# Optimization experiments

Measured on AMD Instinct MI355X. Metric: run time of the kernel, lower is better.

## Reference

```python
import jax, jax.numpy as jnp
import numpy as np

BLOCK_SIZE = 128
N_OUT = 4096
K_IN = 4096


def setup_inputs() -> dict:
    key = jax.random.key(0)
    k_x, k_w, k_s = jax.random.split(key, 3)
    x = jax.random.normal(k_x, (1, 1024, K_IN), dtype=jnp.float32)
    # ternary weights stored as int8 in {-2,-1,0,+1} (zero-point subtracted)
    weight_q = (jax.random.randint(k_w, (N_OUT, K_IN), 0, 4) - 2).astype(jnp.int8)
    n_blocks = K_IN // BLOCK_SIZE
    scales = jax.random.uniform(k_s, (N_OUT, n_blocks), dtype=jnp.float32) * 0.1 + 0.01
    return {"x": x, "weight_q": weight_q, "scales": scales}


def reference(x, weight_q, scales):
    N, K = weight_q.shape
    n_blocks = K // BLOCK_SIZE
    orig_shape = x.shape
    # [tokens, n_blocks, block_size]
    x_blocked = x.reshape(-1, n_blocks, BLOCK_SIZE).astype(jnp.float32)
    # [N, n_blocks, block_size]
    w_blocked = weight_q.reshape(N, n_blocks, BLOCK_SIZE).astype(jnp.float32)
    # per-block partial dot products: [tokens, N, n_blocks]
    raw = jnp.einsum('bki,nki->bnk', x_blocked, w_blocked)
    # apply per-(out_feature, block) scale then reduce over blocks
    out = (raw * scales).sum(axis=-1)  # [tokens, N]
    return out.astype(x.dtype).reshape(*orig_shape[:-1], N)
```

## Files before the change

kernel.cpp:

```cpp
#include <hip/hip_runtime.h>
#include <stdint.h>


#define MM 1024
#define NN 4096
#define KK 4096
#define BK 128

typedef __attribute__((ext_vector_type(4))) int intx4;
typedef __attribute__((ext_vector_type(4))) float floatx4;

typedef const __attribute__((address_space(1))) void global_cvoid;
typedef __attribute__((address_space(3))) void lds_void;

__global__ __launch_bounds__(256) void quant_x(const float* __restrict__ x,
                                               char* __restrict__ xq,
                                               float* __restrict__ qrow) {
    const int m   = blockIdx.x;
    const int tid = threadIdx.x;
    const float* xr = x + (size_t)m * KK;
    floatx4 v[4];
    float amax = 0.f;
#pragma unroll
    for (int c = 0; c < 4; ++c) {
        v[c] = *(const floatx4*)(xr + (c * 256 + tid) * 4);
#pragma unroll
        for (int e = 0; e < 4; ++e) amax = fmaxf(amax, fabsf(v[c][e]));
    }
#pragma unroll
    for (int off = 32; off; off >>= 1) amax = fmaxf(amax, __shfl_down(amax, off));
    __shared__ float wmax[4];
    if ((tid & 63) == 0) wmax[tid >> 6] = amax;
    __syncthreads();
    amax = fmaxf(fmaxf(wmax[0], wmax[1]), fmaxf(wmax[2], wmax[3]));
    amax = fmaxf(amax, 1e-20f);
    const float qinv = 127.0f / amax;
    if (tid == 0) qrow[m] = amax / 127.0f;
#pragma unroll
    for (int c = 0; c < 4; ++c) {
        int p = 0;
#pragma unroll
        for (int e = 0; e < 4; ++e) {
            float r = rintf(v[c][e] * qinv);
            r = fminf(fmaxf(r, -127.f), 127.f);
            p |= ((int)r & 255) << (8 * e);
        }
        *(int*)(xq + (size_t)m * KK + (c * 256 + tid) * 4) = p;
    }
}

__global__ __launch_bounds__(256) void conv_w8(const int* __restrict__ wq,
                                               char* __restrict__ wb) {
    int t = blockIdx.x * 256 + threadIdx.x;
    const intx4* src = (const intx4*)wq + (size_t)t * 4;
    intx4 o;
#pragma unroll
    for (int c = 0; c < 4; ++c) {
        intx4 a = src[c];
        o[c] = (a[0] & 255) | ((a[1] & 255) << 8) | ((a[2] & 255) << 16) | (a[3] << 24);
    }
    *((intx4*)wb + t) = o;
}

__global__ __launch_bounds__(256) void q8_gemm(const char* __restrict__ xq,
                                               const char* __restrict__ wb,
                                               const float* __restrict__ qrow,
                                               const float* __restrict__ scales,
                                               float* __restrict__ out) {
    __shared__ char As[2][128 * BK];
    __shared__ char Bs[2][128 * BK];
    __shared__ float Sl[32 * 128];

    const int tid  = threadIdx.x;
    const int lane = tid & 63;
    const int wave = tid >> 6;
    const int wm   = (wave & 1) * 64;
    const int wn   = (wave >> 1) * 64;
    const int r16  = lane & 15;
    const int quad = lane >> 4;
    const int sw   = r16 & 7;

    const int bid = blockIdx.x;
    const int xcd = bid & 7, loc = bid >> 3;
    const int nT = xcd * 4 + (loc & 3);
    const int mT = loc >> 2;
    const int mBase = mT * 128, nBase = nT * 128;

    const int rg = lane >> 3;
    const int cs = (lane & 7) ^ rg;
    const char* gA = xq + (size_t)(mBase + wave * 32 + rg) * KK + cs * 16;
    const char* gB = wb + (size_t)(nBase + wave * 32 + rg) * KK + cs * 16;
    const int ldsRow = wave * 32;

    floatx4 facc[4][4];
#pragma unroll
    for (int i = 0; i < 4; ++i)
#pragma unroll
        for (int j = 0; j < 4; ++j) facc[i][j] = (floatx4){0.f, 0.f, 0.f, 0.f};

#define STAGE(BUF, SLAB)                                                        \
    {                                                                           \
        _Pragma("unroll")                                                       \
        for (int t = 0; t < 4; ++t) {                                           \
            __builtin_amdgcn_global_load_lds(                                   \
                (global_cvoid*)(gA + (size_t)(t * 8) * KK + (SLAB) * BK),       \
                (lds_void*)&As[BUF][(ldsRow + t * 8) * BK], 16, 0, 0);          \
            __builtin_amdgcn_global_load_lds(                                   \
                (global_cvoid*)(gB + (size_t)(t * 8) * KK + (SLAB) * BK),       \
                (lds_void*)&Bs[BUF][(ldsRow + t * 8) * BK], 16, 0, 0);          \
        }                                                                       \
    }

#define COMPUTE(BUF, SLAB)                                                      \
    {                                                                           \
        intx4 iacc[4][4];                                                       \
        _Pragma("unroll")                                                       \
        for (int kp = 0; kp < 2; ++kp) {                                        \
            intx4 av[4], bv[4];                                                 \
            _Pragma("unroll")                                                   \
            for (int i = 0; i < 4; ++i)                                         \
                av[i] = *(const intx4*)&As[BUF][(wm + i * 16 + r16) * BK +      \
                                               (((kp * 4 + quad) ^ sw) << 4)];  \
            _Pragma("unroll")                                                   \
            for (int j = 0; j < 4; ++j)                                         \
                bv[j] = *(const intx4*)&Bs[BUF][(wn + j * 16 + r16) * BK +      \
                                               (((kp * 4 + quad) ^ sw) << 4)];  \
            _Pragma("unroll")                                                   \
            for (int i = 0; i < 4; ++i)                                         \
                _Pragma("unroll")                                               \
                for (int j = 0; j < 4; ++j)                                     \
                    iacc[i][j] = __builtin_amdgcn_mfma_i32_16x16x64_i8(         \
                        av[i], bv[j], kp ? iacc[i][j] : (intx4){0, 0, 0, 0},    \
                        0, 0, 0);                                               \
        }                                                                       \
        float sf[4];                                                            \
        _Pragma("unroll")                                                       \
        for (int j = 0; j < 4; ++j) sf[j] = Sl[(SLAB) * 128 + wn + j * 16 + r16];\
        _Pragma("unroll")                                                       \
        for (int i = 0; i < 4; ++i)                                             \
            _Pragma("unroll")                                                   \
            for (int j = 0; j < 4; ++j)                                         \
                _Pragma("unroll")                                               \
                for (int r = 0; r < 4; ++r)                                     \
                    facc[i][j][r] += (float)iacc[i][j][r] * sf[j];              \
    }

    STAGE(0, 0)
    for (int t = tid; t < 4096; t += 256) {
        Sl[(t & 31) * 128 + (t >> 5)] = scales[(size_t)(nBase + (t >> 5)) * 32 + (t & 31)];
    }
    __syncthreads();

    const int NIT = KK / BK;
    for (int it = 0; it < NIT; it += 2) {
        if (it + 1 < NIT) STAGE(1, it + 1)
        COMPUTE(0, it)
        __syncthreads();
        if (it + 2 < NIT) STAGE(0, it + 2)
        COMPUTE(1, it + 1)
        __syncthreads();
    }

#pragma unroll
    for (int i = 0; i < 4; ++i) {
        floatx4 qv = *(const floatx4*)(qrow + mBase + wm + i * 16 + quad * 4);
#pragma unroll
        for (int r = 0; r < 4; ++r) {
            int mg = mBase + wm + i * 16 + quad * 4 + r;
            float* orow = out + (size_t)mg * NN + nBase + wn + r16;
#pragma unroll
            for (int j = 0; j < 4; ++j) orow[j * 16] = facc[i][j][r] * qv[r];
        }
    }
#undef STAGE
#undef COMPUTE
}

extern "C" void kernel_launch(void* const* d_in, const int* in_sizes, int n_in,
                              void* d_out, int out_size, void* d_ws, size_t ws_size,
                              hipStream_t stream) {
    const float* x      = (const float*)d_in[0];
    const int*   wq     = (const int*)d_in[1];
    const float* scales = (const float*)d_in[2];
    float*       out    = (float*)d_out;

    char*  xq   = (char*)d_ws;
    float* qrow = (float*)((char*)d_ws + (size_t)MM * KK);
    char*  wb   = (char*)d_ws + (size_t)MM * KK + 4096;

    quant_x<<<MM, 256, 0, stream>>>(x, xq, qrow);
    conv_w8<<<(size_t)NN * KK / 16 / 256, 256, 0, stream>>>(wq, wb);
    q8_gemm<<<256, 256, 0, stream>>>(xq, wb, qrow, scales, out);
}
```

Baseline: 157.8 us.

## Fuse activation quantization, weight packing and GEMM into one cooperative kernel

Merges the three launches (x quantization, int8 weight repacking, int8 MFMA GEMM) into a single cooperative kernel of 256 blocks. Each block first quantizes 4 rows of x (one wave per row, reduced with wave shuffles) and repacks 16 weight rows, then all blocks meet at a grid-wide sync before the GEMM phase. This removes two launch boundaries and their tail gaps, at the cost of a grid barrier and using only 256 blocks for the prep work. It also transposes the LDS scale table to a padded row-major layout with stride 33.

Measured after the change: 234.8 us. 1.49x slower.

```diff
diff --git a/kernel.cpp b/kernel.cpp
--- a/kernel.cpp
+++ b/kernel.cpp
@@ -1,5 +1,8 @@
 #include <hip/hip_runtime.h>
+#include <hip/hip_cooperative_groups.h>
 #include <stdint.h>
+
+namespace cg = cooperative_groups;
 
 
 #define MM 1024
@@ -13,74 +16,75 @@
 typedef const __attribute__((address_space(1))) void global_cvoid;
 typedef __attribute__((address_space(3))) void lds_void;
 
-__global__ __launch_bounds__(256) void quant_x(const float* __restrict__ x,
-                                               char* __restrict__ xq,
-                                               float* __restrict__ qrow) {
-    const int m   = blockIdx.x;
-    const int tid = threadIdx.x;
-    const float* xr = x + (size_t)m * KK;
-    floatx4 v[4];
-    float amax = 0.f;
-#pragma unroll
-    for (int c = 0; c < 4; ++c) {
-        v[c] = *(const floatx4*)(xr + (c * 256 + tid) * 4);
-#pragma unroll
-        for (int e = 0; e < 4; ++e) amax = fmaxf(amax, fabsf(v[c][e]));
-    }
-#pragma unroll
-    for (int off = 32; off; off >>= 1) amax = fmaxf(amax, __shfl_down(amax, off));
-    __shared__ float wmax[4];
-    if ((tid & 63) == 0) wmax[tid >> 6] = amax;
-    __syncthreads();
-    amax = fmaxf(fmaxf(wmax[0], wmax[1]), fmaxf(wmax[2], wmax[3]));
-    amax = fmaxf(amax, 1e-20f);
-    const float qinv = 127.0f / amax;
-    if (tid == 0) qrow[m] = amax / 127.0f;
-#pragma unroll
-    for (int c = 0; c < 4; ++c) {
-        int p = 0;
-#pragma unroll
-        for (int e = 0; e < 4; ++e) {
-            float r = rintf(v[c][e] * qinv);
-            r = fminf(fmaxf(r, -127.f), 127.f);
-            p |= ((int)r & 255) << (8 * e);
-        }
-        *(int*)(xq + (size_t)m * KK + (c * 256 + tid) * 4) = p;
-    }
-}
-
-__global__ __launch_bounds__(256) void conv_w8(const int* __restrict__ wq,
-                                               char* __restrict__ wb) {
-    int t = blockIdx.x * 256 + threadIdx.x;
-    const intx4* src = (const intx4*)wq + (size_t)t * 4;
-    intx4 o;
-#pragma unroll
-    for (int c = 0; c < 4; ++c) {
-        intx4 a = src[c];
-        o[c] = (a[0] & 255) | ((a[1] & 255) << 8) | ((a[2] & 255) << 16) | (a[3] << 24);
-    }
-    *((intx4*)wb + t) = o;
-}
-
-__global__ __launch_bounds__(256) void q8_gemm(const char* __restrict__ xq,
-                                               const char* __restrict__ wb,
-                                               const float* __restrict__ qrow,
-                                               const float* __restrict__ scales,
-                                               float* __restrict__ out) {
+__global__ __launch_bounds__(256, 1) void q2_fused(
+    const float* __restrict__ x, const int* __restrict__ wq,
+    const float* __restrict__ scales, float* __restrict__ out,
+    char* __restrict__ xq, float* __restrict__ qrow, char* __restrict__ wb)
+{
     __shared__ char As[2][128 * BK];
     __shared__ char Bs[2][128 * BK];
-    __shared__ float Sl[32 * 128];
+    __shared__ float Sl[128 * 33];
 
     const int tid  = threadIdx.x;
     const int lane = tid & 63;
     const int wave = tid >> 6;
+    const int bid  = blockIdx.x;
+
+    {
+        const int row = bid * 4 + wave;
+        const float* xr = x + (size_t)row * KK;
+        floatx4 v[16];
+        float amax = 0.f;
+#pragma unroll
+        for (int c = 0; c < 16; ++c) {
+            v[c] = *(const floatx4*)(xr + (size_t)(c * 64 + lane) * 4);
+#pragma unroll
+            for (int e = 0; e < 4; ++e) amax = fmaxf(amax, fabsf(v[c][e]));
+        }
+#pragma unroll
+        for (int off = 32; off; off >>= 1) amax = fmaxf(amax, __shfl_xor(amax, off));
+        amax = fmaxf(amax, 1e-20f);
+        const float qinv = 127.0f / amax;
+        if (lane == 0) qrow[row] = amax / 127.0f;
+        char* xo = xq + (size_t)row * KK;
+#pragma unroll
+        for (int c = 0; c < 16; ++c) {
+            int p = 0;
+#pragma unroll
+            for (int e = 0; e < 4; ++e) {
+                float r = rintf(v[c][e] * qinv);
+                r = fminf(fmaxf(r, -127.f), 127.f);
+                p |= ((int)r & 255) << (8 * e);
+            }
+            *(int*)(xo + (size_t)(c * 64 + lane) * 4) = p;
+        }
+    }
+
+    {
+#pragma unroll 4
+        for (int rr = 0; rr < 16; ++rr) {
+            const size_t base = ((size_t)(bid * 16 + rr)) * KK + (size_t)tid * 16;
+            const intx4* src = (const intx4*)(wq + base);
+            intx4 o;
+#pragma unroll
+            for (int c = 0; c < 4; ++c) {
+                intx4 a = src[c];
+                o[c] = (a[0] & 255) | ((a[1] & 255) << 8) |
+                       ((a[2] & 255) << 16) | (a[3] << 24);
+            }
+            *(intx4*)(wb + base) = o;
+        }
+    }
+
+    __threadfence();
+    cg::this_grid().sync();
+
     const int wm   = (wave & 1) * 64;
     const int wn   = (wave >> 1) * 64;
     const int r16  = lane & 15;
     const int quad = lane >> 4;
     const int sw   = r16 & 7;
 
-    const int bid = blockIdx.x;
     const int xcd = bid & 7, loc = bid >> 3;
     const int nT = xcd * 4 + (loc & 3);
     const int mT = loc >> 2;
@@ -135,7 +139,7 @@
         }                                                                       \
         float sf[4];                                                            \
         _Pragma("unroll")                                                       \
-        for (int j = 0; j < 4; ++j) sf[j] = Sl[(SLAB) * 128 + wn + j * 16 + r16];\
+        for (int j = 0; j < 4; ++j) sf[j] = Sl[(wn + j * 16 + r16) * 33 + (SLAB)];\
         _Pragma("unroll")                                                       \
         for (int i = 0; i < 4; ++i)                                             \
             _Pragma("unroll")                                                   \
@@ -147,7 +151,8 @@
 
     STAGE(0, 0)
     for (int t = tid; t < 4096; t += 256) {
-        Sl[(t & 31) * 128 + (t >> 5)] = scales[(size_t)(nBase + (t >> 5)) * 32 + (t & 31)];
+        int nl = t >> 5, b = t & 31;
+        Sl[nl * 33 + b] = scales[(size_t)(nBase + nl) * 32 + b];
     }
     __syncthreads();
 
@@ -188,7 +193,7 @@
     float* qrow = (float*)((char*)d_ws + (size_t)MM * KK);
     char*  wb   = (char*)d_ws + (size_t)MM * KK + 4096;
 
-    quant_x<<<MM, 256, 0, stream>>>(x, xq, qrow);
-    conv_w8<<<(size_t)NN * KK / 16 / 256, 256, 0, stream>>>(wq, wb);
-    q8_gemm<<<256, 256, 0, stream>>>(xq, wb, qrow, scales, out);
+    void* args[] = {(void*)&x, (void*)&wq, (void*)&scales, (void*)&out,
+                    (void*)&xq, (void*)&qrow, (void*)&wb};
+    hipLaunchCooperativeKernel(q2_fused, dim3(256), dim3(256), args, 0, stream);
 }
```

## Halve GEMM M-tile to 64 and read per-block scales directly from global

Applied to the files above, without the earlier changes.

The int8 GEMM tile shrinks from 128x128 to 64x128, so the grid doubles from 256 to 512 blocks, giving more parallelism across the CUs. Each wave now covers all 64 rows and a 32-column slice. The LDS scale table and its prologue fill loop are gone; each lane loads its two per-slab scales straight from global memory. The cost is less data reuse per tile, so more global traffic for B, and scale loads whose latency lands inside the main loop.

Result: faster. 151.9 us (-3.8%).

```diff
diff --git a/kernel.cpp b/kernel.cpp
--- a/kernel.cpp
+++ b/kernel.cpp
@@ -67,88 +67,86 @@
                                                const float* __restrict__ qrow,
                                                const float* __restrict__ scales,
                                                float* __restrict__ out) {
-    __shared__ char As[2][128 * BK];
+    __shared__ char As[2][64 * BK];
     __shared__ char Bs[2][128 * BK];
-    __shared__ float Sl[32 * 128];
 
     const int tid  = threadIdx.x;
     const int lane = tid & 63;
     const int wave = tid >> 6;
-    const int wm   = (wave & 1) * 64;
-    const int wn   = (wave >> 1) * 64;
     const int r16  = lane & 15;
     const int quad = lane >> 4;
     const int sw   = r16 & 7;
+    const int wn   = wave * 32;
 
     const int bid = blockIdx.x;
     const int xcd = bid & 7, loc = bid >> 3;
     const int nT = xcd * 4 + (loc & 3);
     const int mT = loc >> 2;
-    const int mBase = mT * 128, nBase = nT * 128;
+    const int mBase = mT * 64, nBase = nT * 128;
 
     const int rg = lane >> 3;
     const int cs = (lane & 7) ^ rg;
-    const char* gA = xq + (size_t)(mBase + wave * 32 + rg) * KK + cs * 16;
+    const char* gA = xq + (size_t)(mBase + wave * 16 + rg) * KK + cs * 16;
     const char* gB = wb + (size_t)(nBase + wave * 32 + rg) * KK + cs * 16;
-    const int ldsRow = wave * 32;
+    const int ldsRowA = wave * 16;
+    const int ldsRowB = wave * 32;
 
-    floatx4 facc[4][4];
+    const float* sBase = scales + (size_t)(nBase + wn + r16) * 32;
+
+    floatx4 facc[4][2];
 #pragma unroll
     for (int i = 0; i < 4; ++i)
 #pragma unroll
-        for (int j = 0; j < 4; ++j) facc[i][j] = (floatx4){0.f, 0.f, 0.f, 0.f};
+        for (int j = 0; j < 2; ++j) facc[i][j] = (floatx4){0.f, 0.f, 0.f, 0.f};
 
 #define STAGE(BUF, SLAB)                                                        \
     {                                                                           \
         _Pragma("unroll")                                                       \
-        for (int t = 0; t < 4; ++t) {                                           \
+        for (int t = 0; t < 2; ++t)                                             \
             __builtin_amdgcn_global_load_lds(                                   \
                 (global_cvoid*)(gA + (size_t)(t * 8) * KK + (SLAB) * BK),       \
-                (lds_void*)&As[BUF][(ldsRow + t * 8) * BK], 16, 0, 0);          \
+                (lds_void*)&As[BUF][(ldsRowA + t * 8) * BK], 16, 0, 0);         \
+        _Pragma("unroll")                                                       \
+        for (int t = 0; t < 4; ++t)                                             \
             __builtin_amdgcn_global_load_lds(                                   \
                 (global_cvoid*)(gB + (size_t)(t * 8) * KK + (SLAB) * BK),       \
-                (lds_void*)&Bs[BUF][(ldsRow + t * 8) * BK], 16, 0, 0);          \
-        }                                                                       \
+                (lds_void*)&Bs[BUF][(ldsRowB + t * 8) * BK], 16, 0, 0);         \
     }
 
 #define COMPUTE(BUF, SLAB)                                                      \
     {                                                                           \
-        intx4 iacc[4][4];                                                       \
+        float sf0 = sBase[(SLAB)];                                              \
+        float sf1 = sBase[16 * 32 + (SLAB)];                                    \
+        intx4 iacc[4][2];                                                       \
         _Pragma("unroll")                                                       \
         for (int kp = 0; kp < 2; ++kp) {                                        \
-            intx4 av[4], bv[4];                                                 \
+            intx4 av[4], bv[2];                                                 \
             _Pragma("unroll")                                                   \
             for (int i = 0; i < 4; ++i)                                         \
-                av[i] = *(const intx4*)&As[BUF][(wm + i * 16 + r16) * BK +      \
+                av[i] = *(const intx4*)&As[BUF][(i * 16 + r16) * BK +           \
                                                (((kp * 4 + quad) ^ sw) << 4)];  \
             _Pragma("unroll")                                                   \
-            for (int j = 0; j < 4; ++j)                                         \
+            for (int j = 0; j < 2; ++j)                                         \
                 bv[j] = *(const intx4*)&Bs[BUF][(wn + j * 16 + r16) * BK +      \
                                                (((kp * 4 + quad) ^ sw) << 4)];  \
             _Pragma("unroll")                                                   \
             for (int i = 0; i < 4; ++i)                                         \
                 _Pragma("unroll")                                               \
-                for (int j = 0; j < 4; ++j)                                     \
+                for (int j = 0; j < 2; ++j)                                     \
                     iacc[i][j] = __builtin_amdgcn_mfma_i32_16x16x64_i8(         \
                         av[i], bv[j], kp ? iacc[i][j] : (intx4){0, 0, 0, 0},    \
                         0, 0, 0);                                               \
         }                                                                       \
-        float sf[4];                                                            \
-        _Pragma("unroll")                                                       \
-        for (int j = 0; j < 4; ++j) sf[j] = Sl[(SLAB) * 128 + wn + j * 16 + r16];\
         _Pragma("unroll")                                                       \
         for (int i = 0; i < 4; ++i)                                             \
             _Pragma("unroll")                                                   \
-            for (int j = 0; j < 4; ++j)                                         \
-                _Pragma("unroll")                                               \
-                for (int r = 0; r < 4; ++r)                                     \
-                    facc[i][j][r] += (float)iacc[i][j][r] * sf[j];              \
+            for (int r = 0; r < 4; ++r) {                                       \
+                facc[i][0][r] += (float)iacc[i][0][r] * sf0;                    \
+                facc[i][1][r] += (float)iacc[i][1][r] * sf1;                    \
+            }                                                                   \
     }
 
     STAGE(0, 0)
-    for (int t = tid; t < 4096; t += 256) {
-        Sl[(t & 31) * 128 + (t >> 5)] = scales[(size_t)(nBase + (t >> 5)) * 32 + (t & 31)];
-    }
     __syncthreads();
 
     const int NIT = KK / BK;
@@ -163,13 +161,13 @@
 
 #pragma unroll
     for (int i = 0; i < 4; ++i) {
-        floatx4 qv = *(const floatx4*)(qrow + mBase + wm + i * 16 + quad * 4);
+        floatx4 qv = *(const floatx4*)(qrow + mBase + i * 16 + quad * 4);
 #pragma unroll
         for (int r = 0; r < 4; ++r) {
-            int mg = mBase + wm + i * 16 + quad * 4 + r;
+            int mg = mBase + i * 16 + quad * 4 + r;
             float* orow = out + (size_t)mg * NN + nBase + wn + r16;
 #pragma unroll
-            for (int j = 0; j < 4; ++j) orow[j * 16] = facc[i][j][r] * qv[r];
+            for (int j = 0; j < 2; ++j) orow[j * 16] = facc[i][j][r] * qv[r];
         }
     }
 #undef STAGE
@@ -190,5 +188,5 @@
 
     quant_x<<<MM, 256, 0, stream>>>(x, xq, qrow);
     conv_w8<<<(size_t)NN * KK / 16 / 256, 256, 0, stream>>>(wq, wb);
-    q8_gemm<<<256, 256, 0, stream>>>(xq, wb, qrow, scales, out);
+    q8_gemm<<<(MM / 64) * (NN / 128), 256, 0, stream>>>(xq, wb, qrow, scales, out);
 }
```
